# Kernel tuning notes

Measured on AMD Instinct MI355X. Metric: run time of the kernel, lower is better.

The kernel has to match this reference:

```python
import jax, jax.numpy as jnp
import numpy as np

N_NODES = 100000
N_EDGES = 1600000
D_IN, D_H, D_OUT = 512, 128, 64
BN_EPS = 1e-5


def setup_inputs() -> dict:
    key = jax.random.key(0)
    ks = jax.random.split(key, 8)
    x = jax.random.normal(ks[0], (N_NODES, D_IN), dtype=jnp.float32)
    # COO sparse normalized adjacency
    row = jnp.sort(jax.random.randint(ks[1], (N_EDGES,), 0, N_NODES))
    col = jax.random.randint(ks[2], (N_EDGES,), 0, N_NODES)
    adj_vals = jax.random.uniform(ks[3], (N_EDGES,), dtype=jnp.float32) / 16.0
    # GraphConvolution params (xavier_uniform weight, zero bias)
    lim0 = float(np.sqrt(6.0 / (D_IN + D_H)))
    lim1 = float(np.sqrt(6.0 / (D_H + D_OUT)))
    W0 = jax.random.uniform(ks[4], (D_IN, D_H), minval=-lim0, maxval=lim0, dtype=jnp.float32)
    W1 = jax.random.uniform(ks[5], (D_H, D_OUT), minval=-lim1, maxval=lim1, dtype=jnp.float32)
    b0 = jnp.zeros((D_H,), dtype=jnp.float32)
    b1 = jnp.zeros((D_OUT,), dtype=jnp.float32)
    return {"x": x, "W0": W0, "b0": b0, "W1": W1, "b1": b1,
            "adj_vals": adj_vals, "row": row, "col": col}


def _spmm(vals, row, col, h, n):
    # (sparse adj) @ h : gather source rows, scale by edge value, scatter-add to dest
    return jax.ops.segment_sum(vals[:, None] * h[col], row, num_segments=n)


def reference(x, W0, b0, W1, b1, adj_vals, row, col):
    n = x.shape[0]
    # layer 0: adj @ (x @ W0) + b0  (dropout is identity in eval mode)
    h = _spmm(adj_vals, row, col, x @ W0, n) + b0
    h = jax.nn.relu(h)
    # BatchNorm1d(affine=False, track_running_stats=False): batch stats, biased var
    mean = jnp.mean(h, axis=0)
    var = jnp.mean(jnp.square(h - mean), axis=0)
    h = (h - mean) * jax.lax.rsqrt(var + BN_EPS)
    # layer 1: adj @ (h @ W1) + b1
    return _spmm(adj_vals, row, col, h @ W1, n) + b1
```

## Files before the change

kernel.cpp:

```cpp
#include <hip/hip_runtime.h>
#include <hip/hip_bf16.h>
#include <cstdint>
#include <cstddef>

#define D_IN  512
#define D_H   128
#define D_OUT 64
#define SB    256

typedef __attribute__((ext_vector_type(8))) short bf16x8;
typedef __attribute__((ext_vector_type(4))) float f32x4;

__device__ __forceinline__ float bf2f(unsigned short u) {
  union { unsigned int i; float f; } v; v.i = ((unsigned int)u) << 16; return v.f;
}
__device__ __forceinline__ unsigned short f2bf(float f) {
  union { unsigned int i; float f; } v; v.f = f;
  unsigned int r = v.i + 0x7FFFu + ((v.i >> 16) & 1u);
  return (unsigned short)(r >> 16);
}
__device__ __forceinline__ unsigned int pk_bf16(float a, float b) {
  union { __hip_bfloat162 h; unsigned int u; } cv;
  cv.h = __float22bfloat162_rn(make_float2(a, b));
  return cv.u;
}

#define OFF_RP    0u
#define OFF_W0T   400384u
#define OFF_W1TP  531456u
#define OFF_CVEC  547840u
#define OFF_PSUM  548096u
#define OFF_PSQ   679168u
#define OFF_H     810240u
#define END_H     26410240u
#define END_HW    39210240u

__global__ void k_init(const int* __restrict__ row, int* __restrict__ rp,
                       const float* __restrict__ W0, unsigned short* __restrict__ W0t,
                       int n, int e, int RB) {
  int b = blockIdx.x, t = threadIdx.x;
  if (b < RB) {
    int i = b * 256 + t;
    if (i > n) return;
    int lo = 0, hi = e;
    while (lo < hi) { int mid = (lo + hi) >> 1; if (row[mid] < i) lo = mid + 1; else hi = mid; }
    rp[i] = lo;
  } else {
    int idx = (b - RB) * 256 + t;
    int k = idx & (D_IN - 1);
    int nn = idx >> 9;
    W0t[nn * D_IN + k] = f2bf(W0[k * D_H + nn]);
  }
}

__global__ __launch_bounds__(256) void k_gemm1(const float* __restrict__ A,
                                               const unsigned short* __restrict__ Bt,
                                               unsigned short* __restrict__ C, int M) {
  __shared__ unsigned short Ash[2][4096];
  __shared__ unsigned short Bsh[2][4096];
  const int tid = threadIdx.x, lane = tid & 63, wave = tid >> 6;
  const int wm = (wave >> 1) * 64, wn = (wave & 1) * 64;
  const int m0 = blockIdx.x * 128, quad = lane >> 4, l16 = lane & 15;
  f32x4 acc[4][4] = {};
  int am[2], ak[2];
  const float* aptr[2];
  const unsigned short* bptr[2];
#pragma unroll
  for (int i = 0; i < 2; ++i) {
    int c = tid + i * 256;
    am[i] = c >> 2; ak[i] = c & 3;
    int gm = m0 + am[i]; if (gm >= M) gm = M - 1;
    aptr[i] = A + (size_t)gm * D_IN + ak[i] * 8;
    bptr[i] = Bt + (size_t)am[i] * D_IN + ak[i] * 8;
  }
  f32x4 areg[2][2]; bf16x8 breg[2];
#pragma unroll
  for (int i = 0; i < 2; ++i) {
    areg[i][0] = *(const f32x4*)(aptr[i]);
    areg[i][1] = *(const f32x4*)(aptr[i] + 4);
    breg[i]    = *(const bf16x8*)(bptr[i]);
  }
  const int NIT = D_IN / 32;
  for (int it = 0; it < NIT; ++it) {
    const int buf = it & 1;
    unsigned short* ash = Ash[buf];
    unsigned short* bsh = Bsh[buf];
#pragma unroll
    for (int i = 0; i < 2; ++i) {
      unsigned int pk4[4];
      pk4[0] = pk_bf16(areg[i][0][0], areg[i][0][1]);
      pk4[1] = pk_bf16(areg[i][0][2], areg[i][0][3]);
      pk4[2] = pk_bf16(areg[i][1][0], areg[i][1][1]);
      pk4[3] = pk_bf16(areg[i][1][2], areg[i][1][3]);
      *(uint4*)&ash[(ak[i] * 128 + am[i]) * 8] = *(uint4*)pk4;
      *(bf16x8*)&bsh[(ak[i] * 128 + am[i]) * 8] = breg[i];
    }
    __syncthreads();
    if (it + 1 < NIT) {
      int k0 = (it + 1) * 32;
#pragma unroll
      for (int i = 0; i < 2; ++i) {
        areg[i][0] = *(const f32x4*)(aptr[i] + k0);
        areg[i][1] = *(const f32x4*)(aptr[i] + k0 + 4);
        breg[i]    = *(const bf16x8*)(bptr[i] + k0);
      }
    }
    bf16x8 af[4], bfv[4];
#pragma unroll
    for (int mf = 0; mf < 4; ++mf)
      af[mf] = *(const bf16x8*)&ash[(quad * 128 + (wm + mf * 16 + l16)) * 8];
#pragma unroll
    for (int nf = 0; nf < 4; ++nf)
      bfv[nf] = *(const bf16x8*)&bsh[(quad * 128 + (wn + nf * 16 + l16)) * 8];
#pragma unroll
    for (int mf = 0; mf < 4; ++mf)
#pragma unroll
      for (int nf = 0; nf < 4; ++nf)
        acc[mf][nf] = __builtin_amdgcn_mfma_f32_16x16x32_bf16(af[mf], bfv[nf], acc[mf][nf], 0, 0, 0);
  }
#pragma unroll
  for (int mf = 0; mf < 4; ++mf)
#pragma unroll
    for (int nf = 0; nf < 4; ++nf)
#pragma unroll
      for (int i = 0; i < 4; ++i) {
        int r = m0 + wm + mf * 16 + quad * 4 + i;
        int cc = wn + nf * 16 + l16;
        if (r < M) C[(size_t)r * D_H + cc] = f2bf(acc[mf][nf][i]);
      }
}

__global__ __launch_bounds__(256) void k_spmm1(const unsigned int* __restrict__ xw2,
                                               const float* __restrict__ adj,
                                               const int* __restrict__ col,
                                               const int* __restrict__ rp,
                                               const float* __restrict__ b0,
                                               unsigned int* __restrict__ h2, int n) {
  int node = blockIdx.x * 4 + (threadIdx.x >> 6);
  if (node >= n) return;
  int l = threadIdx.x & 63;
  int e0 = rp[node], e1 = rp[node + 1];
  float a0 = 0.f, a1 = 0.f;
  for (int e = e0; e < e1; e += 8) {
    int ee = e + (l & 7);
    int ec = ee < e1 ? ee : e1 - 1;
    int   cl = col[ec];
    float vl = ee < e1 ? adj[ec] : 0.f;
#pragma unroll
    for (int j = 0; j < 8; ++j) {
      int   cj = __shfl(cl, j, 64);
      float wj = __shfl(vl, j, 64);
      unsigned int p = xw2[(size_t)cj * 64 + l];
      a0 += wj * bf2f((unsigned short)(p & 0xFFFF));
      a1 += wj * bf2f((unsigned short)(p >> 16));
    }
  }
  float r0 = fmaxf(a0 + b0[2 * l], 0.f);
  float r1 = fmaxf(a1 + b0[2 * l + 1], 0.f);
  h2[(size_t)node * 64 + l] = ((unsigned int)f2bf(r1) << 16) | (unsigned int)f2bf(r0);
}

__global__ __launch_bounds__(256) void k_stats(const unsigned int* __restrict__ h2,
                                               float* __restrict__ psum,
                                               float* __restrict__ psq, int n) {
  __shared__ float sA[256], sB[256], qA[256], qB[256];
  int t = threadIdx.x;
  int f2 = t & 63, rg = t >> 6;
  float s0 = 0.f, s1 = 0.f, q0 = 0.f, q1 = 0.f;
  for (int r = blockIdx.x * 4 + rg; r < n; r += gridDim.x * 4) {
    unsigned int p = h2[(size_t)r * 64 + f2];
    float v0 = bf2f((unsigned short)(p & 0xFFFF));
    float v1 = bf2f((unsigned short)(p >> 16));
    s0 += v0; s1 += v1; q0 += v0 * v0; q1 += v1 * v1;
  }
  sA[t] = s0; sB[t] = s1; qA[t] = q0; qB[t] = q1;
  __syncthreads();
  if (t < 64) {
    float S0 = sA[t] + sA[t + 64] + sA[t + 128] + sA[t + 192];
    float S1 = sB[t] + sB[t + 64] + sB[t + 128] + sB[t + 192];
    float Q0 = qA[t] + qA[t + 64] + qA[t + 128] + qA[t + 192];
    float Q1 = qB[t] + qB[t + 64] + qB[t + 128] + qB[t + 192];
    psum[blockIdx.x * 128 + 2 * t]     = S0;
    psum[blockIdx.x * 128 + 2 * t + 1] = S1;
    psq [blockIdx.x * 128 + 2 * t]     = Q0;
    psq [blockIdx.x * 128 + 2 * t + 1] = Q1;
  }
}

__global__ void k_prep2(const float* __restrict__ psum, const float* __restrict__ psq,
                        const float* __restrict__ W1,
                        unsigned short* __restrict__ W1tp, float* __restrict__ cvec, int n) {
  __shared__ float rs[256], rq[256];
  __shared__ float mean_s[128], istd_s[128];
  __shared__ float cpart[256];
  int t = threadIdx.x;
  int f = t & 127, half = t >> 7;
  {
    float s = 0.f, q = 0.f;
#pragma unroll 8
    for (int b = half * (SB / 2); b < (half + 1) * (SB / 2); ++b) {
      s += psum[b * 128 + f]; q += psq[b * 128 + f];
    }
    rs[t] = s; rq[t] = q;
  }
  __syncthreads();
  if (t < 128) {
    float s = rs[t] + rs[t + 128];
    float q = rq[t] + rq[t + 128];
    float m = s / (float)n;
    float var = q / (float)n - m * m;
    if (var < 0.f) var = 0.f;
    mean_s[t] = m;
    istd_s[t] = rsqrtf(var + 1e-5f);
  }
  __syncthreads();
  for (int idx = t; idx < D_OUT * D_H; idx += 256) {
    int nn = idx >> 7, k = idx & 127;
    W1tp[nn * D_H + k] = f2bf(istd_s[k] * W1[k * D_OUT + nn]);
  }
  {
    int o = t & 63, part = t >> 6;
    float a = 0.f;
    for (int k = part * 32; k < part * 32 + 32; ++k)
      a += mean_s[k] * istd_s[k] * W1[k * D_OUT + o];
    cpart[t] = a;
  }
  __syncthreads();
  if (t < D_OUT)
    cvec[t] = -(cpart[t] + cpart[t + 64] + cpart[t + 128] + cpart[t + 192]);
}

__global__ __launch_bounds__(256) void k_gemm2(const unsigned short* __restrict__ A,
                                               const unsigned short* __restrict__ Bt,
                                               const float* __restrict__ cvec,
                                               unsigned short* __restrict__ Cout, int M) {
  __shared__ unsigned short Ash[4096];
  __shared__ unsigned short Bsh[2048];
  const int tid = threadIdx.x, lane = tid & 63, wave = tid >> 6;
  const int wm = wave * 32, m0 = blockIdx.x * 128;
  const int quad = lane >> 4, l16 = lane & 15;
  f32x4 acc[2][4] = {};
  for (int k0 = 0; k0 < D_H; k0 += 32) {
    __syncthreads();
#pragma unroll
    for (int i = 0; i < 2; ++i) {
      int c = tid + i * 256;
      int m = c >> 2, k8 = c & 3;
      int gm = m0 + m; if (gm >= M) gm = M - 1;
      *(bf16x8*)&Ash[(k8 * 128 + m) * 8] = *(const bf16x8*)&A[(size_t)gm * D_H + k0 + k8 * 8];
    }
    {
      int nn = tid >> 2, k8 = tid & 3;
      *(bf16x8*)&Bsh[(k8 * 64 + nn) * 8] = *(const bf16x8*)&Bt[(size_t)nn * D_H + k0 + k8 * 8];
    }
    __syncthreads();
    bf16x8 af[2], bfv[4];
#pragma unroll
    for (int mf = 0; mf < 2; ++mf)
      af[mf] = *(const bf16x8*)&Ash[(quad * 128 + (wm + mf * 16 + l16)) * 8];
#pragma unroll
    for (int nf = 0; nf < 4; ++nf)
      bfv[nf] = *(const bf16x8*)&Bsh[(quad * 64 + (nf * 16 + l16)) * 8];
#pragma unroll
    for (int mf = 0; mf < 2; ++mf)
#pragma unroll
      for (int nf = 0; nf < 4; ++nf)
        acc[mf][nf] = __builtin_amdgcn_mfma_f32_16x16x32_bf16(af[mf], bfv[nf], acc[mf][nf], 0, 0, 0);
  }
#pragma unroll
  for (int mf = 0; mf < 2; ++mf)
#pragma unroll
    for (int nf = 0; nf < 4; ++nf)
#pragma unroll
      for (int i = 0; i < 4; ++i) {
        int r = m0 + wm + mf * 16 + quad * 4 + i;
        int cc = nf * 16 + l16;
        if (r < M) Cout[(size_t)r * 64 + cc] = f2bf(acc[mf][nf][i] + cvec[cc]);
      }
}

__global__ __launch_bounds__(256) void k_spmm2(const unsigned int* __restrict__ hw2,
                                               const float* __restrict__ adj,
                                               const int* __restrict__ col,
                                               const int* __restrict__ rp,
                                               const float* __restrict__ b1,
                                               float2* __restrict__ o2, int n) {
  int node = blockIdx.x * 8 + (threadIdx.x >> 5);
  if (node >= n) return;
  int l = threadIdx.x & 31;
  int e0 = rp[node], e1 = rp[node + 1];
  float a0 = 0.f, a1 = 0.f;
  for (int e = e0; e < e1; e += 8) {
    int ee = e + (l & 7);
    int ec = ee < e1 ? ee : e1 - 1;
    int   cl = col[ec];
    float vl = ee < e1 ? adj[ec] : 0.f;
#pragma unroll
    for (int j = 0; j < 8; ++j) {
      int   cj = __shfl(cl, j, 32);
      float wj = __shfl(vl, j, 32);
      unsigned int p = hw2[(size_t)cj * 32 + l];
      a0 += wj * bf2f((unsigned short)(p & 0xFFFF));
      a1 += wj * bf2f((unsigned short)(p >> 16));
    }
  }
  float2 r; r.x = a0 + b1[2 * l]; r.y = a1 + b1[2 * l + 1];
  o2[(size_t)node * 32 + l] = r;
}

extern "C" void kernel_launch(void* const* d_in, const int* in_sizes, int n_in,
                              void* d_out, int out_size, void* d_ws, size_t ws_size,
                              hipStream_t stream) {
  const float* x   = (const float*)d_in[0];
  const float* W0  = (const float*)d_in[1];
  const float* b0  = (const float*)d_in[2];
  const float* W1  = (const float*)d_in[3];
  const float* b1  = (const float*)d_in[4];
  const float* adj = (const float*)d_in[5];
  const int* row = (const int*)d_in[6];
  const int* col = (const int*)d_in[7];
  const int N = in_sizes[0] / D_IN;
  const int E = in_sizes[5];

  char* ws = (char*)d_ws;
  int*            rp   = (int*)(ws + OFF_RP);
  unsigned short* W0t  = (unsigned short*)(ws + OFF_W0T);
  unsigned short* W1tp = (unsigned short*)(ws + OFF_W1TP);
  float*          cvec = (float*)(ws + OFF_CVEC);
  float*          psum = (float*)(ws + OFF_PSUM);
  float*          psq  = (float*)(ws + OFF_PSQ);
  unsigned short* h    = (unsigned short*)(ws + OFF_H);

  unsigned short* xw = (unsigned short*)d_out;
  const bool hw_in_ws = (ws_size >= (size_t)END_HW);
  unsigned short* hwp  = hw_in_ws ? (unsigned short*)(ws + END_H) : (unsigned short*)d_out;
  float*          outd = hw_in_ws ? (float*)d_out                 : (float*)(ws + OFF_H);

  const int RB = (N + 1 + 255) / 256;
  const int TB = (D_IN * D_H) / 256;
  k_init<<<RB + TB, 256, 0, stream>>>(row, rp, W0, W0t, N, E, RB);
  k_gemm1<<<(N + 127) / 128, 256, 0, stream>>>(x, W0t, xw, N);
  k_spmm1<<<(N + 3) / 4, 256, 0, stream>>>((const unsigned int*)xw, adj, col, rp, b0,
                                           (unsigned int*)h, N);
  k_stats<<<SB, 256, 0, stream>>>((const unsigned int*)h, psum, psq, N);
  k_prep2<<<1, 256, 0, stream>>>(psum, psq, W1, W1tp, cvec, N);
  k_gemm2<<<(N + 127) / 128, 256, 0, stream>>>(h, W1tp, cvec, hwp, N);
  k_spmm2<<<(N + 7) / 8, 256, 0, stream>>>((const unsigned int*)hwp, adj, col, rp, b1,
                                           (float2*)outd, N);
  if (!hw_in_ws) {
    hipMemcpyAsync(d_out, outd, (size_t)N * D_OUT * sizeof(float),
                   hipMemcpyDeviceToDevice, stream);
  }
}
```

Measured before the change: 478.0 us.

## Fuse BN stats into SpMM, fold prep into GEMM2, split SpMM by feature slices

The row-pointer search moves into the GEMM1 launch as extra blocks. BatchNorm statistics are now accumulated inside spmm1 with atomics into 64 slots, which removes the separate k_stats kernel. The k_prep2 work (mean, istd, scaled W1, bias vector) is recomputed in every GEMM2 block, so one launch and one round trip disappear. Both SpMMs are restructured so each block handles one 16-column feature slice across 16 nodes, with 4 edges unrolled per iteration. The change aims to cut launch count and improve gather locality per pass. In exchange, edge indices are re-read once per pass and every GEMM2 block redoes the prep arithmetic.

```diff
diff --git a/kernel.cpp b/kernel.cpp
--- a/kernel.cpp
+++ b/kernel.cpp
@@ -6,7 +6,7 @@
 #define D_IN  512
 #define D_H   128
 #define D_OUT 64
-#define SB    256
+#define SB    64
 
 typedef __attribute__((ext_vector_type(8))) short bf16x8;
 typedef __attribute__((ext_vector_type(4))) float f32x4;
@@ -25,42 +25,55 @@
   return cv.u;
 }
 
+#define ACC2(P, W) { unsigned int _p = (P); \
+    union { unsigned int i; float f; } _lo, _hi; \
+    _lo.i = _p << 16; _hi.i = _p & 0xFFFF0000u; \
+    a0 += (W) * _lo.f; a1 += (W) * _hi.f; }
+
 #define OFF_RP    0u
 #define OFF_W0T   400384u
-#define OFF_W1TP  531456u
-#define OFF_CVEC  547840u
 #define OFF_PSUM  548096u
 #define OFF_PSQ   679168u
 #define OFF_H     810240u
 #define END_H     26410240u
-#define END_HW    39210240u
-
-__global__ void k_init(const int* __restrict__ row, int* __restrict__ rp,
-                       const float* __restrict__ W0, unsigned short* __restrict__ W0t,
-                       int n, int e, int RB) {
-  int b = blockIdx.x, t = threadIdx.x;
-  if (b < RB) {
-    int i = b * 256 + t;
-    if (i > n) return;
-    int lo = 0, hi = e;
-    while (lo < hi) { int mid = (lo + hi) >> 1; if (row[mid] < i) lo = mid + 1; else hi = mid; }
-    rp[i] = lo;
-  } else {
-    int idx = (b - RB) * 256 + t;
-    int k = idx & (D_IN - 1);
-    int nn = idx >> 9;
-    W0t[nn * D_IN + k] = f2bf(W0[k * D_H + nn]);
-  }
+#define OFF_XW    39210240u
+#define END_XW    64810240u
+
+__global__ void k_init(const float* __restrict__ W0, unsigned short* __restrict__ W0t) {
+  int idx = blockIdx.x * 256 + threadIdx.x;
+  int k = idx & (D_IN - 1);
+  int nn = idx >> 9;
+  W0t[nn * D_IN + k] = f2bf(W0[k * D_H + nn]);
 }
 
 __global__ __launch_bounds__(256) void k_gemm1(const float* __restrict__ A,
                                                const unsigned short* __restrict__ Bt,
-                                               unsigned short* __restrict__ C, int M) {
+                                               unsigned short* __restrict__ C,
+                                               const int* __restrict__ row,
+                                               int* __restrict__ rp,
+                                               float* __restrict__ psum,
+                                               float* __restrict__ psq,
+                                               int M, int E, int GB, int RB) {
+  int b = blockIdx.x;
+  if (b >= GB) {
+    int bb = b - GB;
+    if (bb < RB) {
+      int i = bb * 256 + threadIdx.x;
+      if (i <= M) {
+        int lo = 0, hi = E;
+        while (lo < hi) { int mid = (lo + hi) >> 1; if (row[mid] < i) lo = mid + 1; else hi = mid; }
+        rp[i] = lo;
+      }
+    } else {
+      for (int i = threadIdx.x; i < SB * 128; i += 256) { psum[i] = 0.f; psq[i] = 0.f; }
+    }
+    return;
+  }
   __shared__ unsigned short Ash[2][4096];
   __shared__ unsigned short Bsh[2][4096];
   const int tid = threadIdx.x, lane = tid & 63, wave = tid >> 6;
   const int wm = (wave >> 1) * 64, wn = (wave & 1) * 64;
-  const int m0 = blockIdx.x * 128, quad = lane >> 4, l16 = lane & 15;
+  const int m0 = b * 128, quad = lane >> 4, l16 = lane & 15;
   f32x4 acc[4][4] = {};
   int am[2], ak[2];
   const float* aptr[2];
@@ -135,108 +148,114 @@
                                                const int* __restrict__ col,
                                                const int* __restrict__ rp,
                                                const float* __restrict__ b0,
-                                               unsigned int* __restrict__ h2, int n) {
-  int node = blockIdx.x * 4 + (threadIdx.x >> 6);
-  if (node >= n) return;
-  int l = threadIdx.x & 63;
-  int e0 = rp[node], e1 = rp[node + 1];
-  float a0 = 0.f, a1 = 0.f;
-  for (int e = e0; e < e1; e += 8) {
-    int ee = e + (l & 7);
-    int ec = ee < e1 ? ee : e1 - 1;
-    int   cl = col[ec];
-    float vl = ee < e1 ? adj[ec] : 0.f;
-#pragma unroll
-    for (int j = 0; j < 8; ++j) {
-      int   cj = __shfl(cl, j, 64);
-      float wj = __shfl(vl, j, 64);
-      unsigned int p = xw2[(size_t)cj * 64 + l];
-      a0 += wj * bf2f((unsigned short)(p & 0xFFFF));
-      a1 += wj * bf2f((unsigned short)(p >> 16));
-    }
-  }
-  float r0 = fmaxf(a0 + b0[2 * l], 0.f);
-  float r1 = fmaxf(a1 + b0[2 * l + 1], 0.f);
-  h2[(size_t)node * 64 + l] = ((unsigned int)f2bf(r1) << 16) | (unsigned int)f2bf(r0);
-}
-
-__global__ __launch_bounds__(256) void k_stats(const unsigned int* __restrict__ h2,
+                                               unsigned int* __restrict__ h2,
                                                float* __restrict__ psum,
-                                               float* __restrict__ psq, int n) {
-  __shared__ float sA[256], sB[256], qA[256], qB[256];
-  int t = threadIdx.x;
-  int f2 = t & 63, rg = t >> 6;
-  float s0 = 0.f, s1 = 0.f, q0 = 0.f, q1 = 0.f;
-  for (int r = blockIdx.x * 4 + rg; r < n; r += gridDim.x * 4) {
-    unsigned int p = h2[(size_t)r * 64 + f2];
-    float v0 = bf2f((unsigned short)(p & 0xFFFF));
-    float v1 = bf2f((unsigned short)(p >> 16));
-    s0 += v0; s1 += v1; q0 += v0 * v0; q1 += v1 * v1;
-  }
-  sA[t] = s0; sB[t] = s1; qA[t] = q0; qB[t] = q1;
+                                               float* __restrict__ psq,
+                                               int n, int PB) {
+  __shared__ float sE[4][16], sO[4][16], qE[4][16], qO[4][16];
+  const int t = threadIdx.x, wave = t >> 6, l = t & 63;
+  const int g = l >> 4, l16 = l & 15;
+  const int pass = blockIdx.x / PB;
+  const int nb = blockIdx.x - pass * PB;
+  const int node = nb * 16 + wave * 4 + g;
+  const unsigned int* src = xw2 + pass * 16 + l16;
+  float r0 = 0.f, r1 = 0.f;
+  if (node < n) {
+    const int e0 = rp[node], e1 = rp[node + 1];
+    float a0 = 0.f, a1 = 0.f;
+    for (int e = e0; e < e1; e += 4) {
+      int i1 = e + 1 < e1 ? e + 1 : e;
+      int i2 = e + 2 < e1 ? e + 2 : e;
+      int i3 = e + 3 < e1 ? e + 3 : e;
+      int   c0 = col[e],  c1 = col[i1], c2 = col[i2], c3 = col[i3];
+      float w0 = adj[e];
+      float w1 = e + 1 < e1 ? adj[i1] : 0.f;
+      float w2 = e + 2 < e1 ? adj[i2] : 0.f;
+      float w3 = e + 3 < e1 ? adj[i3] : 0.f;
+      unsigned int p0 = src[(size_t)c0 * 64];
+      unsigned int p1 = src[(size_t)c1 * 64];
+      unsigned int p2 = src[(size_t)c2 * 64];
+      unsigned int p3 = src[(size_t)c3 * 64];
+      ACC2(p0, w0); ACC2(p1, w1); ACC2(p2, w2); ACC2(p3, w3);
+    }
+    float2 bb = *(const float2*)(b0 + pass * 32 + 2 * l16);
+    r0 = fmaxf(a0 + bb.x, 0.f);
+    r1 = fmaxf(a1 + bb.y, 0.f);
+    h2[(size_t)node * 64 + pass * 16 + l16] =
+        ((unsigned int)f2bf(r1) << 16) | (unsigned int)f2bf(r0);
+  }
+  float s0 = r0, s1 = r1, q0 = r0 * r0, q1 = r1 * r1;
+  s0 += __shfl_xor(s0, 16, 64); s0 += __shfl_xor(s0, 32, 64);
+  s1 += __shfl_xor(s1, 16, 64); s1 += __shfl_xor(s1, 32, 64);
+  q0 += __shfl_xor(q0, 16, 64); q0 += __shfl_xor(q0, 32, 64);
+  q1 += __shfl_xor(q1, 16, 64); q1 += __shfl_xor(q1, 32, 64);
+  if (g == 0) { sE[wave][l16] = s0; sO[wave][l16] = s1;
+                qE[wave][l16] = q0; qO[wave][l16] = q1; }
   __syncthreads();
-  if (t < 64) {
-    float S0 = sA[t] + sA[t + 64] + sA[t + 128] + sA[t + 192];
-    float S1 = sB[t] + sB[t + 64] + sB[t + 128] + sB[t + 192];
-    float Q0 = qA[t] + qA[t + 64] + qA[t + 128] + qA[t + 192];
-    float Q1 = qB[t] + qB[t + 64] + qB[t + 128] + qB[t + 192];
-    psum[blockIdx.x * 128 + 2 * t]     = S0;
-    psum[blockIdx.x * 128 + 2 * t + 1] = S1;
-    psq [blockIdx.x * 128 + 2 * t]     = Q0;
-    psq [blockIdx.x * 128 + 2 * t + 1] = Q1;
-  }
-}
-
-__global__ void k_prep2(const float* __restrict__ psum, const float* __restrict__ psq,
-                        const float* __restrict__ W1,
-                        unsigned short* __restrict__ W1tp, float* __restrict__ cvec, int n) {
+  if (t < 16) {
+    float S0 = sE[0][t] + sE[1][t] + sE[2][t] + sE[3][t];
+    float S1 = sO[0][t] + sO[1][t] + sO[2][t] + sO[3][t];
+    float Q0 = qE[0][t] + qE[1][t] + qE[2][t] + qE[3][t];
+    float Q1 = qO[0][t] + qO[1][t] + qO[2][t] + qO[3][t];
+    int base = (blockIdx.x & (SB - 1)) * 128 + pass * 32 + 2 * t;
+    atomicAdd(&psum[base],     S0);
+    atomicAdd(&psum[base + 1], S1);
+    atomicAdd(&psq[base],      Q0);
+    atomicAdd(&psq[base + 1],  Q1);
+  }
+}
+
+__global__ __launch_bounds__(256) void k_gemm2(const unsigned short* __restrict__ A,
+                                               const float* __restrict__ psum,
+                                               const float* __restrict__ psq,
+                                               const float* __restrict__ W1,
+                                               unsigned short* __restrict__ Cout,
+                                               int M, int n) {
   __shared__ float rs[256], rq[256];
   __shared__ float mean_s[128], istd_s[128];
-  __shared__ float cpart[256];
-  int t = threadIdx.x;
-  int f = t & 127, half = t >> 7;
+  __shared__ float cvec_s[64];
+  __shared__ unsigned short BF[1024 * 8];
+  __shared__ unsigned short Ash[4096];
+  const int tid = threadIdx.x, lane = tid & 63, wave = tid >> 6;
   {
+    int f = tid & 127, hh = tid >> 7;
     float s = 0.f, q = 0.f;
 #pragma unroll 8
-    for (int b = half * (SB / 2); b < (half + 1) * (SB / 2); ++b) {
-      s += psum[b * 128 + f]; q += psq[b * 128 + f];
-    }
-    rs[t] = s; rq[t] = q;
+    for (int bsl = hh * (SB / 2); bsl < (hh + 1) * (SB / 2); ++bsl) {
+      s += psum[bsl * 128 + f]; q += psq[bsl * 128 + f];
+    }
+    rs[tid] = s; rq[tid] = q;
   }
   __syncthreads();
-  if (t < 128) {
-    float s = rs[t] + rs[t + 128];
-    float q = rq[t] + rq[t + 128];
+  if (tid < 128) {
+    float s = rs[tid] + rs[tid + 128];
+    float q = rq[tid] + rq[tid + 128];
     float m = s / (float)n;
     float var = q / (float)n - m * m;
     if (var < 0.f) var = 0.f;
-    mean_s[t] = m;
-    istd_s[t] = rsqrtf(var + 1e-5f);
+    mean_s[tid] = m;
+    istd_s[tid] = rsqrtf(var + 1e-5f);
   }
   __syncthreads();
-  for (int idx = t; idx < D_OUT * D_H; idx += 256) {
-    int nn = idx >> 7, k = idx & 127;
-    W1tp[nn * D_H + k] = f2bf(istd_s[k] * W1[k * D_OUT + nn]);
+  for (int idx = tid; idx < 1024; idx += 256) {
+    int kk8 = idx >> 6, nn = idx & 63;
+    unsigned short* dst = &BF[idx * 8];
+#pragma unroll
+    for (int j = 0; j < 8; ++j) {
+      int k = kk8 * 8 + j;
+      dst[j] = f2bf(istd_s[k] * W1[k * D_OUT + nn]);
+    }
   }
   {
-    int o = t & 63, part = t >> 6;
+    int o = tid & 63, part = tid >> 6;
     float a = 0.f;
     for (int k = part * 32; k < part * 32 + 32; ++k)
       a += mean_s[k] * istd_s[k] * W1[k * D_OUT + o];
-    cpart[t] = a;
+    rs[tid] = a;
   }
   __syncthreads();
-  if (t < D_OUT)
-    cvec[t] = -(cpart[t] + cpart[t + 64] + cpart[t + 128] + cpart[t + 192]);
-}
-
-__global__ __launch_bounds__(256) void k_gemm2(const unsigned short* __restrict__ A,
-                                               const unsigned short* __restrict__ Bt,
-                                               const float* __restrict__ cvec,
-                                               unsigned short* __restrict__ Cout, int M) {
-  __shared__ unsigned short Ash[4096];
-  __shared__ unsigned short Bsh[2048];
-  const int tid = threadIdx.x, lane = tid & 63, wave = tid >> 6;
+  if (tid < D_OUT)
+    cvec_s[tid] = -(rs[tid] + rs[tid + 64] + rs[tid + 128] + rs[tid + 192]);
   const int wm = wave * 32, m0 = blockIdx.x * 128;
   const int quad = lane >> 4, l16 = lane & 15;
   f32x4 acc[2][4] = {};
@@ -249,10 +268,6 @@
       int gm = m0 + m; if (gm >= M) gm = M - 1;
       *(bf16x8*)&Ash[(k8 * 128 + m) * 8] = *(const bf16x8*)&A[(size_t)gm * D_H + k0 + k8 * 8];
     }
-    {
-      int nn = tid >> 2, k8 = tid & 3;
-      *(bf16x8*)&Bsh[(k8 * 64 + nn) * 8] = *(const bf16x8*)&Bt[(size_t)nn * D_H + k0 + k8 * 8];
-    }
     __syncthreads();
     bf16x8 af[2], bfv[4];
 #pragma unroll
@@ -260,7 +275,7 @@
       af[mf] = *(const bf16x8*)&Ash[(quad * 128 + (wm + mf * 16 + l16)) * 8];
 #pragma unroll
     for (int nf = 0; nf < 4; ++nf)
-      bfv[nf] = *(const bf16x8*)&Bsh[(quad * 64 + (nf * 16 + l16)) * 8];
+      bfv[nf] = *(const bf16x8*)&BF[(((k0 >> 3) + quad) * 64 + nf * 16 + l16) * 8];
 #pragma unroll
     for (int mf = 0; mf < 2; ++mf)
 #pragma unroll
@@ -275,7 +290,7 @@
       for (int i = 0; i < 4; ++i) {
         int r = m0 + wm + mf * 16 + quad * 4 + i;
         int cc = nf * 16 + l16;
-        if (r < M) Cout[(size_t)r * 64 + cc] = f2bf(acc[mf][nf][i] + cvec[cc]);
+        if (r < M) Cout[(size_t)r * 64 + cc] = f2bf(acc[mf][nf][i] + cvec_s[cc]);
       }
 }
 
@@ -284,28 +299,35 @@
                                                const int* __restrict__ col,
                                                const int* __restrict__ rp,
                                                const float* __restrict__ b1,
-                                               float2* __restrict__ o2, int n) {
-  int node = blockIdx.x * 8 + (threadIdx.x >> 5);
+                                               float* __restrict__ outp,
+                                               int n, int PB) {
+  const int t = threadIdx.x, wave = t >> 6, l = t & 63;
+  const int g = l >> 4, l16 = l & 15;
+  const int pass = blockIdx.x / PB;
+  const int nb = blockIdx.x - pass * PB;
+  const int node = nb * 16 + wave * 4 + g;
   if (node >= n) return;
-  int l = threadIdx.x & 31;
-  int e0 = rp[node], e1 = rp[node + 1];
+  const unsigned int* src = hw2 + pass * 16 + l16;
+  const int e0 = rp[node], e1 = rp[node + 1];
   float a0 = 0.f, a1 = 0.f;
-  for (int e = e0; e < e1; e += 8) {
-    int ee = e + (l & 7);
-    int ec = ee < e1 ? ee : e1 - 1;
-    int   cl = col[ec];
-    float vl = ee < e1 ? adj[ec] : 0.f;
-#pragma unroll
-    for (int j = 0; j < 8; ++j) {
-      int   cj = __shfl(cl, j, 32);
-      float wj = __shfl(vl, j, 32);
-      unsigned int p = hw2[(size_t)cj * 32 + l];
-      a0 += wj * bf2f((unsigned short)(p & 0xFFFF));
-      a1 += wj * bf2f((unsigned short)(p >> 16));
-    }
-  }
-  float2 r; r.x = a0 + b1[2 * l]; r.y = a1 + b1[2 * l + 1];
-  o2[(size_t)node * 32 + l] = r;
+  for (int e = e0; e < e1; e += 4) {
+    int i1 = e + 1 < e1 ? e + 1 : e;
+    int i2 = e + 2 < e1 ? e + 2 : e;
+    int i3 = e + 3 < e1 ? e + 3 : e;
+    int   c0 = col[e],  c1 = col[i1], c2 = col[i2], c3 = col[i3];
+    float w0 = adj[e];
+    float w1 = e + 1 < e1 ? adj[i1] : 0.f;
+    float w2 = e + 2 < e1 ? adj[i2] : 0.f;
+    float w3 = e + 3 < e1 ? adj[i3] : 0.f;
+    unsigned int p0 = src[(size_t)c0 * 32];
+    unsigned int p1 = src[(size_t)c1 * 32];
+    unsigned int p2 = src[(size_t)c2 * 32];
+    unsigned int p3 = src[(size_t)c3 * 32];
+    ACC2(p0, w0); ACC2(p1, w1); ACC2(p2, w2); ACC2(p3, w3);
+  }
+  float2 bb = *(const float2*)(b1 + pass * 32 + 2 * l16);
+  float2 r; r.x = a0 + bb.x; r.y = a1 + bb.y;
+  *(float2*)(outp + (size_t)node * 64 + pass * 32 + 2 * l16) = r;
 }
 
 extern "C" void kernel_launch(void* const* d_in, const int* in_sizes, int n_in,
@@ -325,30 +347,23 @@
   char* ws = (char*)d_ws;
   int*            rp   = (int*)(ws + OFF_RP);
   unsigned short* W0t  = (unsigned short*)(ws + OFF_W0T);
-  unsigned short* W1tp = (unsigned short*)(ws + OFF_W1TP);
-  float*          cvec = (float*)(ws + OFF_CVEC);
   float*          psum = (float*)(ws + OFF_PSUM);
   float*          psq  = (float*)(ws + OFF_PSQ);
   unsigned short* h    = (unsigned short*)(ws + OFF_H);
 
-  unsigned short* xw = (unsigned short*)d_out;
-  const bool hw_in_ws = (ws_size >= (size_t)END_HW);
-  unsigned short* hwp  = hw_in_ws ? (unsigned short*)(ws + END_H) : (unsigned short*)d_out;
-  float*          outd = hw_in_ws ? (float*)d_out                 : (float*)(ws + OFF_H);
-
+  const bool big_ws = (ws_size >= (size_t)END_XW);
+  unsigned short* xw   = big_ws ? (unsigned short*)(ws + OFF_XW) : (unsigned short*)d_out;
+  unsigned short* hwp  = big_ws ? (unsigned short*)(ws + END_H)  : (unsigned short*)d_out;
+  float*          outd = (float*)d_out;
+
+  const int GB = (N + 127) / 128;
   const int RB = (N + 1 + 255) / 256;
-  const int TB = (D_IN * D_H) / 256;
-  k_init<<<RB + TB, 256, 0, stream>>>(row, rp, W0, W0t, N, E, RB);
-  k_gemm1<<<(N + 127) / 128, 256, 0, stream>>>(x, W0t, xw, N);
-  k_spmm1<<<(N + 3) / 4, 256, 0, stream>>>((const unsigned int*)xw, adj, col, rp, b0,
-                                           (unsigned int*)h, N);
-  k_stats<<<SB, 256, 0, stream>>>((const unsigned int*)h, psum, psq, N);
-  k_prep2<<<1, 256, 0, stream>>>(psum, psq, W1, W1tp, cvec, N);
-  k_gemm2<<<(N + 127) / 128, 256, 0, stream>>>(h, W1tp, cvec, hwp, N);
-  k_spmm2<<<(N + 7) / 8, 256, 0, stream>>>((const unsigned int*)hwp, adj, col, rp, b1,
-                                           (float2*)outd, N);
-  if (!hw_in_ws) {
-    hipMemcpyAsync(d_out, outd, (size_t)N * D_OUT * sizeof(float),
-                   hipMemcpyDeviceToDevice, stream);
-  }
-}
+  const int PB = (N + 15) / 16;
+  k_init<<<(D_IN * D_H) / 256, 256, 0, stream>>>(W0, W0t);
+  k_gemm1<<<GB + RB + 1, 256, 0, stream>>>(x, W0t, xw, row, rp, psum, psq, N, E, GB, RB);
+  k_spmm1<<<4 * PB, 256, 0, stream>>>((const unsigned int*)xw, adj, col, rp, b0,
+                                      (unsigned int*)h, psum, psq, N, PB);
+  k_gemm2<<<GB, 256, 0, stream>>>(h, psum, psq, W1, hwp, N, N);
+  k_spmm2<<<2 * PB, 256, 0, stream>>>((const unsigned int*)hwp, adj, col, rp, b1,
+                                      outd, N, PB);
+}
```

Measured after the change: 503.4 us. 1.05x slower.
